# Performance work log

Hardware: AMD Instinct MI355X
Metric: run time of the kernel (lower is better)

## Reference

```python
import jax, jax.numpy as jnp
import numpy as np

N_HEAD = 8


def setup_inputs() -> dict:
    key = jax.random.key(0)
    k1, k2, k3, k4 = jax.random.split(key, 4)
    B, C, T, F = 2, 128, 512, 512
    x = jax.random.normal(k1, (B, C, T, F), dtype=jnp.float32)
    Wq = jax.random.normal(k2, (F, F), dtype=jnp.float32) * (F ** -0.5)
    bq = jax.random.normal(k3, (F,), dtype=jnp.float32) * 0.02
    Wk = jax.random.normal(k4, (F, F), dtype=jnp.float32) * (F ** -0.5)
    return {"x": x, "Wq": Wq, "bq": bq, "Wk": Wk}


def reference(x, Wq, bq, Wk):
    B, C, T, F = x.shape
    H = N_HEAD
    d = F // H
    # v: permute (0,1,3,2) -> (B,C,F,T), flatten -> (B,C,F*T)
    v = jnp.transpose(x, (0, 1, 3, 2)).reshape(B, C, F * T)
    # mean over permuted dim 3 (== original T axis)
    xm = jnp.mean(x, axis=2)  # (B,C,F)
    q = xm @ Wq.T + bq        # (B,C,F)
    k = xm @ Wk.T             # (B,C,F)
    scale = d ** (-0.25)
    qh = q.reshape(B, C, H, d).transpose(0, 2, 1, 3) * scale   # (B,H,C,d)
    kh = k.reshape(B, C, H, d).transpose(0, 2, 3, 1) * scale   # (B,H,d,C)
    dv = (F * T) // H
    vh = v.reshape(B, C, H, dv).transpose(0, 2, 1, 3)          # (B,H,C,dv)
    qk = jnp.einsum('bhcd,bhdk->bhck', qh, kh)                 # (B,H,C,C)
    w = jax.nn.softmax(qk.astype(jnp.float32), axis=-1).astype(qh.dtype)
    wv = jnp.einsum('bhck,bhkd->bhcd', w, vh)                  # (B,H,C,dv)
    wv = wv.transpose(0, 2, 1, 3).reshape(B, C, F * T).reshape(B, C, F, T)
    # inverse permute (0,1,3,2) -> (B,C,T,F)
    return jnp.transpose(wv, (0, 1, 3, 2))
```

## Files before the change

### kernel.cpp

```cpp
#include <hip/hip_runtime.h>
#include <hip/hip_bf16.h>

#define CC 128
#define TT 512
#define FF 512
#define CS (TT * FF)

typedef __attribute__((ext_vector_type(8))) short short8;
typedef __attribute__((ext_vector_type(4))) float f32x4;

__device__ __forceinline__ unsigned short f2b(float f) {
    union { float f; unsigned u; } a; a.f = f;
    unsigned r = a.u + 0x7fffu + ((a.u >> 16) & 1u);
    return (unsigned short)(r >> 16);
}

__global__ __launch_bounds__(1024) void mean_kernel(const float* __restrict__ x,
                                                    float* __restrict__ xm) {
    int bc = blockIdx.x;
    int q4  = threadIdx.x & 127;
    int par = threadIdx.x >> 7;
    const f32x4* xp = (const f32x4*)(x + (size_t)bc * CS);
    int kb = bc + (par << 3);
    f32x4 s0 = (f32x4){0.f,0.f,0.f,0.f}, s1 = s0, s2 = s0, s3 = s0;
    #pragma unroll 4
    for (int k = 0; k < 64; k += 4) {
        int k0 = (kb + k)     & 63;
        int k1 = (kb + k + 1) & 63;
        int k2 = (kb + k + 2) & 63;
        int k3 = (kb + k + 3) & 63;
        f32x4 a = __builtin_nontemporal_load(xp + (par + 8 * k0) * 128 + q4);
        f32x4 b = __builtin_nontemporal_load(xp + (par + 8 * k1) * 128 + q4);
        f32x4 c = __builtin_nontemporal_load(xp + (par + 8 * k2) * 128 + q4);
        f32x4 d = __builtin_nontemporal_load(xp + (par + 8 * k3) * 128 + q4);
        s0 += a; s1 += b; s2 += c; s3 += d;
    }
    s0 += s1; s2 += s3; s0 += s2;
    __shared__ f32x4 part[1024];
    part[threadIdx.x] = s0;
    __syncthreads();
    if (par == 0) {
        const float inv = 1.0f / (float)TT;
        f32x4 acc = (f32x4){0.f,0.f,0.f,0.f};
        #pragma unroll
        for (int j = 0; j < 8; ++j) acc += part[q4 + 128 * j];
        acc *= inv;
        *(f32x4*)((float*)xm + (size_t)bc * 512 + q4 * 4) = acc;
    }
}

__global__ void qk_kernel(const float* __restrict__ xm, const float* __restrict__ Wq,
                          const float* __restrict__ bq, const float* __restrict__ Wk,
                          float* __restrict__ qo, float* __restrict__ ko) {
    __shared__ float xs[32][65];
    __shared__ float wqs[32][65];
    __shared__ float wks[32][65];
    int ft = blockIdx.x, rt = blockIdx.y;
    int t = threadIdx.x;
    int tx = t & 15, ty = t >> 4;
    float qa[2][2] = {{0.f,0.f},{0.f,0.f}}, ka[2][2] = {{0.f,0.f},{0.f,0.f}};
    for (int kc = 0; kc < 512; kc += 64) {
        __syncthreads();
        for (int i = t; i < 2048; i += 256) {
            int r = i >> 6, cc2 = i & 63;
            xs[r][cc2]  = xm[(rt * 32 + r) * 512 + kc + cc2];
            wqs[r][cc2] = Wq[(ft * 32 + r) * 512 + kc + cc2];
            wks[r][cc2] = Wk[(ft * 32 + r) * 512 + kc + cc2];
        }
        __syncthreads();
        #pragma unroll 8
        for (int kk = 0; kk < 64; ++kk) {
            float x0 = xs[ty*2][kk],  x1 = xs[ty*2+1][kk];
            float a0 = wqs[tx*2][kk], a1 = wqs[tx*2+1][kk];
            float b0 = wks[tx*2][kk], b1 = wks[tx*2+1][kk];
            qa[0][0] += x0*a0; qa[0][1] += x0*a1;
            qa[1][0] += x1*a0; qa[1][1] += x1*a1;
            ka[0][0] += x0*b0; ka[0][1] += x0*b1;
            ka[1][0] += x1*b0; ka[1][1] += x1*b1;
        }
    }
    #pragma unroll
    for (int i = 0; i < 2; ++i) {
        int r = rt * 32 + ty * 2 + i;
        #pragma unroll
        for (int j = 0; j < 2; ++j) {
            int f = ft * 32 + tx * 2 + j;
            qo[r * 512 + f] = qa[i][j] + bq[f];
            ko[r * 512 + f] = ka[i][j];
        }
    }
}

__global__ void attn_w_kernel(const float* __restrict__ q, const float* __restrict__ k,
                              float* __restrict__ w) {
    int idx = blockIdx.x;
    int bh = idx >> 7, c = idx & 127;
    int b = bh >> 3, h = bh & 7;
    int f0 = h * 64;
    __shared__ float qv[64];
    __shared__ float wmax[2];
    __shared__ float wsum[2];
    int t = threadIdx.x;
    if (t < 64) qv[t] = q[((b * CC + c) * FF) + f0 + t];
    __syncthreads();
    const float* kp = k + ((size_t)(b * CC + t) * FF) + f0;
    float acc = 0.f;
    #pragma unroll
    for (int j = 0; j < 64; j += 4) {
        float4 kv = *(const float4*)(kp + j);
        acc += qv[j] * kv.x + qv[j+1] * kv.y + qv[j+2] * kv.z + qv[j+3] * kv.w;
    }
    float logit = acc * 0.125f;
    float m = logit;
    #pragma unroll
    for (int o = 32; o >= 1; o >>= 1) m = fmaxf(m, __shfl_xor(m, o));
    if ((t & 63) == 0) wmax[t >> 6] = m;
    __syncthreads();
    m = fmaxf(wmax[0], wmax[1]);
    float e = expf(logit - m);
    float s = e;
    #pragma unroll
    for (int o = 32; o >= 1; o >>= 1) s += __shfl_xor(s, o);
    if ((t & 63) == 0) wsum[t >> 6] = s;
    __syncthreads();
    s = wsum[0] + wsum[1];
    w[((size_t)bh * 128 + c) * 128 + t] = e / s;
}

__global__ __launch_bounds__(256, 2) void wv_kernel(const float* __restrict__ x,
                                                    const float* __restrict__ wmat,
                                                    float* __restrict__ out) {
    int bh = blockIdx.y;
    int b = bh >> 3, h = bh & 7;
    __shared__ unsigned short Wl[128 * 128];

    {
        int tid = threadIdx.x;
        int c = tid & 127, half = tid >> 7;
        const float* wp = wmat + ((size_t)bh * 128 + c) * 128 + half * 64;
        unsigned swz = (unsigned)((c & 7) << 4);
        char* base = (char*)Wl + c * 256;
        #pragma unroll
        for (int j = 0; j < 8; ++j) {
            f32x4 v0 = *(const f32x4*)(wp + j * 8);
            f32x4 v1 = *(const f32x4*)(wp + j * 8 + 4);
            short8 pk;
            pk[0] = (short)f2b(v0[0]); pk[1] = (short)f2b(v0[1]);
            pk[2] = (short)f2b(v0[2]); pk[3] = (short)f2b(v0[3]);
            pk[4] = (short)f2b(v1[0]); pk[5] = (short)f2b(v1[1]);
            pk[6] = (short)f2b(v1[2]); pk[7] = (short)f2b(v1[3]);
            *(short8*)(base + (((unsigned)(half * 128 + j * 16)) ^ swz)) = pk;
        }
    }
    __syncthreads();

    int ln  = threadIdx.x & 63;
    int wv_ = threadIdx.x >> 6;
    int nco = ln & 15;
    int kg  = ln >> 4;
    int arow = ln & 15;
    unsigned aswz = (unsigned)((arow & 7) << 4);
    const float* xb = x + (size_t)b * CC * CS;
    float* ob = out + (size_t)b * CC * CS;

    for (int it = 0; it < 8; ++it) {
        int ti = blockIdx.x * 4 + wv_ + it * 128;
        int col0 = ti << 5;
        int t = col0 >> 6;
        int fbase = (h << 6) + (col0 & 63);
        const float* xc = xb + (size_t)t * FF + fbase + nco + (size_t)(kg * 8) * CS;

        f32x4 acc[8][2];
        #pragma unroll
        for (int m = 0; m < 8; ++m) {
            acc[m][0] = (f32x4){0.f, 0.f, 0.f, 0.f};
            acc[m][1] = (f32x4){0.f, 0.f, 0.f, 0.f};
        }

        #pragma unroll
        for (int ks = 0; ks < 4; ++ks) {
            const float* p0 = xc + (size_t)(ks * 32) * CS;
            short8 bf[2];
            #pragma unroll
            for (int nt = 0; nt < 2; ++nt) {
                const float* p = p0 + nt * 16;
                float v0 = __builtin_nontemporal_load(p);
                float v1 = __builtin_nontemporal_load(p + (size_t)1 * CS);
                float v2 = __builtin_nontemporal_load(p + (size_t)2 * CS);
                float v3 = __builtin_nontemporal_load(p + (size_t)3 * CS);
                float v4 = __builtin_nontemporal_load(p + (size_t)4 * CS);
                float v5 = __builtin_nontemporal_load(p + (size_t)5 * CS);
                float v6 = __builtin_nontemporal_load(p + (size_t)6 * CS);
                float v7 = __builtin_nontemporal_load(p + (size_t)7 * CS);
                short8 bb;
                bb[0] = (short)f2b(v0); bb[1] = (short)f2b(v1);
                bb[2] = (short)f2b(v2); bb[3] = (short)f2b(v3);
                bb[4] = (short)f2b(v4); bb[5] = (short)f2b(v5);
                bb[6] = (short)f2b(v6); bb[7] = (short)f2b(v7);
                bf[nt] = bb;
            }
            #pragma unroll
            for (int m = 0; m < 8; ++m) {
                unsigned abyte = (unsigned)((m * 16 + arow) * 256)
                               + (((unsigned)((ks * 4 + kg) << 4)) ^ aswz);
                short8 af = *(const short8*)((const char*)Wl + abyte);
                acc[m][0] = __builtin_amdgcn_mfma_f32_16x16x32_bf16(af, bf[0], acc[m][0], 0, 0, 0);
                acc[m][1] = __builtin_amdgcn_mfma_f32_16x16x32_bf16(af, bf[1], acc[m][1], 0, 0, 0);
            }
        }

        float* o0 = ob + (size_t)t * FF + fbase + nco;
        #pragma unroll
        for (int m = 0; m < 8; ++m) {
            int crow = m * 16 + kg * 4;
            #pragma unroll
            for (int nt = 0; nt < 2; ++nt) {
                float* op = o0 + (size_t)crow * CS + nt * 16;
                #pragma unroll
                for (int j = 0; j < 4; ++j) {
                    __builtin_nontemporal_store(acc[m][nt][j], op + (size_t)j * CS);
                }
            }
        }
    }
}

extern "C" void kernel_launch(void* const* d_in, const int* in_sizes, int n_in,
                              void* d_out, int out_size, void* d_ws, size_t ws_size,
                              hipStream_t stream) {
    (void)in_sizes; (void)n_in; (void)out_size; (void)ws_size;
    const float* x  = (const float*)d_in[0];
    const float* Wq = (const float*)d_in[1];
    const float* bq = (const float*)d_in[2];
    const float* Wk = (const float*)d_in[3];
    float* out = (float*)d_out;

    float* ws = (float*)d_ws;
    float* xm = ws;
    float* q  = ws + 131072;
    float* k  = ws + 262144;
    float* w  = ws + 393216;

    hipLaunchKernelGGL(mean_kernel,   dim3(256),    dim3(1024), 0, stream, x, xm);
    hipLaunchKernelGGL(qk_kernel,     dim3(16, 8),  dim3(256),  0, stream, xm, Wq, bq, Wk, q, k);
    hipLaunchKernelGGL(attn_w_kernel, dim3(2048),   dim3(128),  0, stream, q, k, w);
    hipLaunchKernelGGL(wv_kernel,     dim3(32, 16), dim3(256),  0, stream, x, w, out);
}
```

Baseline: 222.8 us.

## Precompute bf16 copy of x in mean pass and feed it to wv kernel

The mean kernel now also converts x to bf16 and writes it to the workspace, and the wv kernel reads this bf16 copy instead of converting fp32 on the fly. This removes the second fp32 read and the per-element conversion in wv, but adds a 128 MiB write and read of the bf16 buffer, so total memory traffic is roughly unchanged. The path is used only when the workspace is large enough; otherwise it falls back to the original kernels.

```diff
diff --git a/kernel.cpp b/kernel.cpp
--- a/kernel.cpp
+++ b/kernel.cpp
@@ -8,6 +8,7 @@
 
 typedef __attribute__((ext_vector_type(8))) short short8;
 typedef __attribute__((ext_vector_type(4))) float f32x4;
+typedef __attribute__((ext_vector_type(4))) unsigned short u16x4;
 
 __device__ __forceinline__ unsigned short f2b(float f) {
     union { float f; unsigned u; } a; a.f = f;
@@ -15,12 +16,14 @@
     return (unsigned short)(r >> 16);
 }
 
-__global__ __launch_bounds__(1024) void mean_kernel(const float* __restrict__ x,
-                                                    float* __restrict__ xm) {
+__global__ __launch_bounds__(1024) void cvtmean_kernel(const float* __restrict__ x,
+                                                       unsigned short* __restrict__ xb,
+                                                       float* __restrict__ xm) {
     int bc = blockIdx.x;
     int q4  = threadIdx.x & 127;
     int par = threadIdx.x >> 7;
     const f32x4* xp = (const f32x4*)(x + (size_t)bc * CS);
+    unsigned long long* bp = (unsigned long long*)(xb + (size_t)bc * CS);
     int kb = bc + (par << 3);
     f32x4 s0 = (f32x4){0.f,0.f,0.f,0.f}, s1 = s0, s2 = s0, s3 = s0;
     #pragma unroll 4
@@ -34,6 +37,15 @@
         f32x4 c = __builtin_nontemporal_load(xp + (par + 8 * k2) * 128 + q4);
         f32x4 d = __builtin_nontemporal_load(xp + (par + 8 * k3) * 128 + q4);
         s0 += a; s1 += b; s2 += c; s3 += d;
+        union { u16x4 v; unsigned long long u; } pa, pb, pc, pd;
+        pa.v = (u16x4){ f2b(a[0]), f2b(a[1]), f2b(a[2]), f2b(a[3]) };
+        pb.v = (u16x4){ f2b(b[0]), f2b(b[1]), f2b(b[2]), f2b(b[3]) };
+        pc.v = (u16x4){ f2b(c[0]), f2b(c[1]), f2b(c[2]), f2b(c[3]) };
+        pd.v = (u16x4){ f2b(d[0]), f2b(d[1]), f2b(d[2]), f2b(d[3]) };
+        bp[(par + 8 * k0) * 128 + q4] = pa.u;
+        bp[(par + 8 * k1) * 128 + q4] = pb.u;
+        bp[(par + 8 * k2) * 128 + q4] = pc.u;
+        bp[(par + 8 * k3) * 128 + q4] = pd.u;
     }
     s0 += s1; s2 += s3; s0 += s2;
     __shared__ f32x4 part[1024];
@@ -127,9 +139,9 @@
     w[((size_t)bh * 128 + c) * 128 + t] = e / s;
 }
 
-__global__ __launch_bounds__(256, 2) void wv_kernel(const float* __restrict__ x,
-                                                    const float* __restrict__ wmat,
-                                                    float* __restrict__ out) {
+__global__ __launch_bounds__(256, 2) void wv5_kernel(const unsigned short* __restrict__ xb,
+                                                     const float* __restrict__ wmat,
+                                                     float* __restrict__ out) {
     int bh = blockIdx.y;
     int b = bh >> 3, h = bh & 7;
     __shared__ unsigned short Wl[128 * 128];
@@ -160,7 +172,7 @@
     int kg  = ln >> 4;
     int arow = ln & 15;
     unsigned aswz = (unsigned)((arow & 7) << 4);
-    const float* xb = x + (size_t)b * CC * CS;
+    const unsigned short* xbb = xb + (size_t)b * CC * CS;
     float* ob = out + (size_t)b * CC * CS;
 
     for (int it = 0; it < 8; ++it) {
@@ -168,7 +180,7 @@
         int col0 = ti << 5;
         int t = col0 >> 6;
         int fbase = (h << 6) + (col0 & 63);
-        const float* xc = xb + (size_t)t * FF + fbase + nco + (size_t)(kg * 8) * CS;
+        const unsigned short* xc = xbb + (size_t)t * FF + fbase + nco + (size_t)(kg * 8) * CS;
 
         f32x4 acc[8][2];
         #pragma unroll
@@ -179,24 +191,20 @@
 
         #pragma unroll
         for (int ks = 0; ks < 4; ++ks) {
-            const float* p0 = xc + (size_t)(ks * 32) * CS;
+            const unsigned short* p0 = xc + (size_t)(ks * 32) * CS;
             short8 bf[2];
             #pragma unroll
             for (int nt = 0; nt < 2; ++nt) {
-                const float* p = p0 + nt * 16;
-                float v0 = __builtin_nontemporal_load(p);
-                float v1 = __builtin_nontemporal_load(p + (size_t)1 * CS);
-                float v2 = __builtin_nontemporal_load(p + (size_t)2 * CS);
-                float v3 = __builtin_nontemporal_load(p + (size_t)3 * CS);
-                float v4 = __builtin_nontemporal_load(p + (size_t)4 * CS);
-                float v5 = __builtin_nontemporal_load(p + (size_t)5 * CS);
-                float v6 = __builtin_nontemporal_load(p + (size_t)6 * CS);
-                float v7 = __builtin_nontemporal_load(p + (size_t)7 * CS);
+                const unsigned short* p = p0 + nt * 16;
                 short8 bb;
-                bb[0] = (short)f2b(v0); bb[1] = (short)f2b(v1);
-                bb[2] = (short)f2b(v2); bb[3] = (short)f2b(v3);
-                bb[4] = (short)f2b(v4); bb[5] = (short)f2b(v5);
-                bb[6] = (short)f2b(v6); bb[7] = (short)f2b(v7);
+                bb[0] = (short)p[0];
+                bb[1] = (short)p[(size_t)1 * CS];
+                bb[2] = (short)p[(size_t)2 * CS];
+                bb[3] = (short)p[(size_t)3 * CS];
+                bb[4] = (short)p[(size_t)4 * CS];
+                bb[5] = (short)p[(size_t)5 * CS];
+                bb[6] = (short)p[(size_t)6 * CS];
+                bb[7] = (short)p[(size_t)7 * CS];
                 bf[nt] = bb;
             }
             #pragma unroll
@@ -225,24 +233,151 @@
     }
 }
 
+__global__ __launch_bounds__(256, 2) void wv_kernel(const float* __restrict__ x,
+                                                    const float* __restrict__ wmat,
+                                                    float* __restrict__ out) {
+    int bh = blockIdx.y;
+    int b = bh >> 3, h = bh & 7;
+    __shared__ unsigned short Wl[128 * 128];
+    {
+        int tid = threadIdx.x;
+        int c = tid & 127, half = tid >> 7;
+        const float* wp = wmat + ((size_t)bh * 128 + c) * 128 + half * 64;
+        unsigned swz = (unsigned)((c & 7) << 4);
+        char* base = (char*)Wl + c * 256;
+        #pragma unroll
+        for (int j = 0; j < 8; ++j) {
+            f32x4 v0 = *(const f32x4*)(wp + j * 8);
+            f32x4 v1 = *(const f32x4*)(wp + j * 8 + 4);
+            short8 pk;
+            pk[0] = (short)f2b(v0[0]); pk[1] = (short)f2b(v0[1]);
+            pk[2] = (short)f2b(v0[2]); pk[3] = (short)f2b(v0[3]);
+            pk[4] = (short)f2b(v1[0]); pk[5] = (short)f2b(v1[1]);
+            pk[6] = (short)f2b(v1[2]); pk[7] = (short)f2b(v1[3]);
+            *(short8*)(base + (((unsigned)(half * 128 + j * 16)) ^ swz)) = pk;
+        }
+    }
+    __syncthreads();
+    int ln  = threadIdx.x & 63;
+    int wv_ = threadIdx.x >> 6;
+    int nco = ln & 15;
+    int kg  = ln >> 4;
+    int arow = ln & 15;
+    unsigned aswz = (unsigned)((arow & 7) << 4);
+    const float* xbp = x + (size_t)b * CC * CS;
+    float* ob = out + (size_t)b * CC * CS;
+    for (int it = 0; it < 8; ++it) {
+        int ti = blockIdx.x * 4 + wv_ + it * 128;
+        int col0 = ti << 5;
+        int t = col0 >> 6;
+        int fbase = (h << 6) + (col0 & 63);
+        const float* xc = xbp + (size_t)t * FF + fbase + nco + (size_t)(kg * 8) * CS;
+        f32x4 acc[8][2];
+        #pragma unroll
+        for (int m = 0; m < 8; ++m) {
+            acc[m][0] = (f32x4){0.f, 0.f, 0.f, 0.f};
+            acc[m][1] = (f32x4){0.f, 0.f, 0.f, 0.f};
+        }
+        #pragma unroll
+        for (int ks = 0; ks < 4; ++ks) {
+            const float* p0 = xc + (size_t)(ks * 32) * CS;
+            short8 bf[2];
+            #pragma unroll
+            for (int nt = 0; nt < 2; ++nt) {
+                const float* p = p0 + nt * 16;
+                short8 bb;
+                #pragma unroll
+                for (int j = 0; j < 8; ++j) bb[j] = (short)f2b(p[(size_t)j * CS]);
+                bf[nt] = bb;
+            }
+            #pragma unroll
+            for (int m = 0; m < 8; ++m) {
+                unsigned abyte = (unsigned)((m * 16 + arow) * 256)
+                               + (((unsigned)((ks * 4 + kg) << 4)) ^ aswz);
+                short8 af = *(const short8*)((const char*)Wl + abyte);
+                acc[m][0] = __builtin_amdgcn_mfma_f32_16x16x32_bf16(af, bf[0], acc[m][0], 0, 0, 0);
+                acc[m][1] = __builtin_amdgcn_mfma_f32_16x16x32_bf16(af, bf[1], acc[m][1], 0, 0, 0);
+            }
+        }
+        float* o0 = ob + (size_t)t * FF + fbase + nco;
+        #pragma unroll
+        for (int m = 0; m < 8; ++m) {
+            int crow = m * 16 + kg * 4;
+            #pragma unroll
+            for (int nt = 0; nt < 2; ++nt) {
+                float* op = o0 + (size_t)crow * CS + nt * 16;
+                #pragma unroll
+                for (int j = 0; j < 4; ++j)
+                    __builtin_nontemporal_store(acc[m][nt][j], op + (size_t)j * CS);
+            }
+        }
+    }
+}
+
+__global__ __launch_bounds__(1024) void mean_kernel(const float* __restrict__ x,
+                                                    float* __restrict__ xm) {
+    int bc = blockIdx.x;
+    int q4  = threadIdx.x & 127;
+    int par = threadIdx.x >> 7;
+    const f32x4* xp = (const f32x4*)(x + (size_t)bc * CS);
+    int kb = bc + (par << 3);
+    f32x4 s0 = (f32x4){0.f,0.f,0.f,0.f}, s1 = s0, s2 = s0, s3 = s0;
+    #pragma unroll 4
+    for (int k = 0; k < 64; k += 4) {
+        int k0 = (kb + k) & 63, k1 = (kb + k + 1) & 63;
+        int k2 = (kb + k + 2) & 63, k3 = (kb + k + 3) & 63;
+        s0 += __builtin_nontemporal_load(xp + (par + 8 * k0) * 128 + q4);
+        s1 += __builtin_nontemporal_load(xp + (par + 8 * k1) * 128 + q4);
+        s2 += __builtin_nontemporal_load(xp + (par + 8 * k2) * 128 + q4);
+        s3 += __builtin_nontemporal_load(xp + (par + 8 * k3) * 128 + q4);
+    }
+    s0 += s1; s2 += s3; s0 += s2;
+    __shared__ f32x4 part[1024];
+    part[threadIdx.x] = s0;
+    __syncthreads();
+    if (par == 0) {
+        const float inv = 1.0f / (float)TT;
+        f32x4 acc = (f32x4){0.f,0.f,0.f,0.f};
+        #pragma unroll
+        for (int j = 0; j < 8; ++j) acc += part[q4 + 128 * j];
+        acc *= inv;
+        *(f32x4*)((float*)xm + (size_t)bc * 512 + q4 * 4) = acc;
+    }
+}
+
 extern "C" void kernel_launch(void* const* d_in, const int* in_sizes, int n_in,
                               void* d_out, int out_size, void* d_ws, size_t ws_size,
                               hipStream_t stream) {
-    (void)in_sizes; (void)n_in; (void)out_size; (void)ws_size;
+    (void)in_sizes; (void)n_in; (void)out_size;
     const float* x  = (const float*)d_in[0];
     const float* Wq = (const float*)d_in[1];
     const float* bq = (const float*)d_in[2];
     const float* Wk = (const float*)d_in[3];
     float* out = (float*)d_out;
 
-    float* ws = (float*)d_ws;
-    float* xm = ws;
-    float* q  = ws + 131072;
-    float* k  = ws + 262144;
-    float* w  = ws + 393216;
-
-    hipLaunchKernelGGL(mean_kernel,   dim3(256),    dim3(1024), 0, stream, x, xm);
-    hipLaunchKernelGGL(qk_kernel,     dim3(16, 8),  dim3(256),  0, stream, xm, Wq, bq, Wk, q, k);
-    hipLaunchKernelGGL(attn_w_kernel, dim3(2048),   dim3(128),  0, stream, q, k, w);
-    hipLaunchKernelGGL(wv_kernel,     dim3(32, 16), dim3(256),  0, stream, x, w, out);
-}
+    const size_t XB_BYTES = (size_t)2 * CC * CS * sizeof(unsigned short);
+    const size_t NEED = XB_BYTES + 4ull * (131072 + 131072 + 131072 + 262144);
+
+    if (ws_size >= NEED) {
+        unsigned short* xbuf = (unsigned short*)d_ws;
+        float* tail = (float*)((char*)d_ws + XB_BYTES);
+        float* xm = tail;
+        float* q  = tail + 131072;
+        float* k  = tail + 262144;
+        float* w  = tail + 393216;
+        hipLaunchKernelGGL(cvtmean_kernel, dim3(256),    dim3(1024), 0, stream, x, xbuf, xm);
+        hipLaunchKernelGGL(qk_kernel,      dim3(16, 8),  dim3(256),  0, stream, xm, Wq, bq, Wk, q, k);
+        hipLaunchKernelGGL(attn_w_kernel,  dim3(2048),   dim3(128),  0, stream, q, k, w);
+        hipLaunchKernelGGL(wv5_kernel,     dim3(32, 16), dim3(256),  0, stream, xbuf, w, out);
+    } else {
+        float* ws = (float*)d_ws;
+        float* xm = ws;
+        float* q  = ws + 131072;
+        float* k  = ws + 262144;
+        float* w  = ws + 393216;
+        hipLaunchKernelGGL(mean_kernel,    dim3(256),    dim3(1024), 0, stream, x, xm);
+        hipLaunchKernelGGL(qk_kernel,      dim3(16, 8),  dim3(256),  0, stream, xm, Wq, bq, Wk, q, k);
+        hipLaunchKernelGGL(attn_w_kernel,  dim3(2048),   dim3(128),  0, stream, q, k, w);
+        hipLaunchKernelGGL(wv_kernel,      dim3(32, 16), dim3(256),  0, stream, x, w, out);
+    }
+}
```

Result: faster. 209.1 us, median of 2 (-6.1%).
